# Performance work log

Measured on AMD Instinct MI355X. Metric: run time of the kernel, lower is better.

Reference implementation:

```python
import jax, jax.numpy as jnp
import numpy as np

BZ, IN_DIM, STATE_DIM, OUT_DIM, L = 16, 512, 512, 512, 2048
INIT_SCALE = 0.5


def setup_inputs() -> dict:
    key = jax.random.key(0)
    k_u, k_a, k_b, k_c = jax.random.split(key, 4)
    u = jax.random.normal(k_u, (BZ, IN_DIM, L), dtype=jnp.float32)
    A_unconstrained = jax.random.normal(k_a, (STATE_DIM,), dtype=jnp.float32) * 0.1
    B = jax.random.normal(k_b, (STATE_DIM, IN_DIM), dtype=jnp.float32) * INIT_SCALE / np.sqrt(IN_DIM)
    C = jax.random.normal(k_c, (OUT_DIM, STATE_DIM), dtype=jnp.float32) * INIT_SCALE / np.sqrt(STATE_DIM)
    D = jnp.zeros((OUT_DIM, IN_DIM), dtype=jnp.float32)
    h0 = jnp.zeros((STATE_DIM,), dtype=jnp.float32)
    return {"u": u, "A_unconstrained": A_unconstrained, "B": B, "C": C, "D": D, "h0": h0}


def reference(u, A_unconstrained, B, C, D, h0):
    # u: (Bz, input_dim, L)
    Bz = u.shape[0]
    A_diag = -jax.nn.softplus(A_unconstrained)  # (S,)
    # Time-invariant input projection, batched over all timesteps: (L, Bz, S)
    Bu = jnp.einsum('bil,si->lbs', u, B)

    state0 = jnp.broadcast_to(h0[None, :], (Bz, h0.shape[0]))

    def step(state, bu_t):
        x_t = state * A_diag[None, :] + bu_t  # (Bz, S)
        return x_t, x_t

    _, xs = jax.lax.scan(step, state0, Bu)  # xs: (L, Bz, S)

    # Output projection: y_t = C x_t + D u_t  -> (Bz, out, L)
    Y = jnp.einsum('lbs,os->bol', xs, C) + jnp.einsum('bil,oi->bol', u, D)
    return Y
```

## Files before the change

### kernel.cpp

```cpp
#include <hip/hip_runtime.h>
#include <math.h>

typedef __bf16 bf16;
typedef __bf16 bf16x2 __attribute__((ext_vector_type(2)));
typedef __bf16 bf16x4 __attribute__((ext_vector_type(4)));
typedef __bf16 bf16x8 __attribute__((ext_vector_type(8)));
typedef float  f32x4  __attribute__((ext_vector_type(4)));

#define BZd 16
#define INd 512
#define Sd  512
#define Od  512
#define Ld  2048
#define CLd 128
#define NCd (Ld / CLd)

__device__ __forceinline__ int keyf(int r) { return (r & 3) ^ ((r >> 2) & 3); }

__global__ __launch_bounds__(256) void prep_all(const float* __restrict__ B,
                                                const float* __restrict__ C,
                                                const float* __restrict__ D,
                                                const float* __restrict__ Au,
                                                bf16* __restrict__ Bb, bf16* __restrict__ Cb,
                                                bf16* __restrict__ Db, float* __restrict__ A_diag,
                                                int* __restrict__ dfa) {
    __shared__ int sred[4];
    int bid = blockIdx.x;
    if (bid == 768) {
        #pragma unroll
        for (int r = 0; r < 2; ++r) {
            int ss = threadIdx.x + r * 256;
            float x = Au[ss];
            float sp = fmaxf(x, 0.0f) + log1pf(expf(-fabsf(x)));
            A_diag[ss] = -sp;
        }
        return;
    }
    int which = bid >> 8, lb = bid & 255;
    const float* src = which == 0 ? B : (which == 1 ? C : D);
    bf16* dst = which == 0 ? Bb : (which == 1 ? Cb : Db);
    int i = lb * 256 + threadIdx.x;
    f32x4 v = *(const f32x4*)&src[(size_t)i * 4];
    bf16x4 o = { (bf16)v[0], (bf16)v[1], (bf16)v[2], (bf16)v[3] };
    *(bf16x4*)&dst[(size_t)i * 4] = o;
    if (which == 2) {
        int nz = (v[0] != 0.f) | (v[1] != 0.f) | (v[2] != 0.f) | (v[3] != 0.f);
        unsigned long long bl = __ballot(nz);
        int wv = threadIdx.x >> 6;
        if ((threadIdx.x & 63) == 0) sred[wv] = (bl != 0ull);
        __syncthreads();
        if (threadIdx.x == 0) dfa[lb] = sred[0] | sred[1] | sred[2] | sred[3];
    }
}

template<int AREG, int SCAN>
__global__ __launch_bounds__(512, 2) void gemm8p(
    const bf16* __restrict__ Abf, size_t aBS,
    const float* __restrict__ Uf, size_t uBS,
    const bf16* __restrict__ Bbf, size_t bBS,
    const bf16* __restrict__ Dbf,
    const int* __restrict__ dfa,
    const float* __restrict__ A_diag, float* __restrict__ cePtr,
    void* __restrict__ OutV, size_t oBS, int ldOut,
    int NX, int NY)
{
    constexpr int RS   = AREG ? 40 : 32;
    constexpr int ASZ  = 256 * RS;
    constexpr int SLOT = ASZ + 256 * 32;
    __shared__ bf16 lds[4 * SLOT];

    const int tid = threadIdx.x;
    const int lane = tid & 63, w = tid >> 6;

    int nwg = gridDim.x, bid = blockIdx.x;
    int cpx = nwg >> 3;
    int swz = (bid & 7) * cpx + (bid >> 3);
    int pb = NX * NY;
    int b  = swz / pb;
    int r0 = swz - b * pb;
    int by = r0 / NX;
    int bx = r0 - by * NX;

    const int wm = w >> 2, wn = w & 3;
    const int fr = lane & 15, g = lane >> 4;
    const int iq = tid & 7, lq = tid >> 3;

    const bf16*  Ab = AREG ? nullptr : (Abf + (size_t)b * aBS + (size_t)(by * 256) * 512);
    const float* Ub = Uf ? (Uf + (size_t)b * uBS) : nullptr;
    const bf16*  Bp = Bbf + (size_t)b * bBS + (size_t)(bx * 256) * 512;

    int extra = 0;
    if (!AREG && dfa) {
        int4 f = ((const int4*)dfa)[lane];
        extra = __any((f.x | f.y | f.z | f.w) != 0) ? 1 : 0;
    }

    f32x4 acc[8][4];
    #pragma unroll
    for (int i = 0; i < 8; ++i)
        #pragma unroll
        for (int j = 0; j < 4; ++j)
            acc[i][j] = (f32x4){0.f, 0.f, 0.f, 0.f};

    f32x4 areg[4];

    #define GLD16(srcP, dstElem) __builtin_amdgcn_global_load_lds( \
        (const __attribute__((address_space(1))) void*)(srcP), \
        (__attribute__((address_space(3))) void*)&lds[dstElem], 16, 0, 0)

    auto gldA = [&](int U) {
        #pragma unroll
        for (int rb = 0; rb < 2; ++rb) {
            int row = rb * 128 + (tid >> 2);
            int cs = (tid & 3) ^ keyf(row);
            GLD16(Ab + (size_t)row * 512 + U * 32 + cs * 8,
                  (U & 3) * SLOT + (rb * 128 + w * 16) * 32);
        }
    };
    auto gldB = [&](int U) {
        #pragma unroll
        for (int rb = 0; rb < 2; ++rb) {
            int row = rb * 128 + (tid >> 2);
            int cs = (tid & 3) ^ keyf(row);
            GLD16(Bp + (size_t)row * 512 + U * 32 + cs * 8,
                  (U & 3) * SLOT + ASZ + (rb * 128 + w * 16) * 32);
        }
    };
    auto issueA = [&](int U) {
        #pragma unroll
        for (int d = 0; d < 4; ++d)
            areg[d] = *(const f32x4*)&Ub[(size_t)(U * 32 + iq * 4 + d) * Ld + by * 256 + lq * 4];
    };
    auto writeA = [&](int U) {
        bf16* As = &lds[(U & 3) * SLOT];
        #pragma unroll
        for (int dl = 0; dl < 4; ++dl) {
            int r = lq * 4 + dl;
            bf16x4 wv = { (bf16)areg[0][dl], (bf16)areg[1][dl], (bf16)areg[2][dl], (bf16)areg[3][dl] };
            *(bf16x4*)&As[r * RS + iq * 4] = wv;
        }
    };
    auto readFrags = [&](int slot, bf16x8* avf, bf16x8* bvf) {
        const bf16* As = &lds[slot * SLOT];
        const bf16* Bs = &lds[slot * SLOT + ASZ];
        #pragma unroll
        for (int i = 0; i < 8; ++i) {
            int R = wm * 128 + i * 16 + fr;
            if (AREG) avf[i] = *(const bf16x8*)&As[R * RS + g * 8];
            else      avf[i] = *(const bf16x8*)&As[R * RS + (g ^ keyf(R)) * 8];
        }
        #pragma unroll
        for (int j = 0; j < 4; ++j) {
            int R = wn * 64 + j * 16 + fr;
            bvf[j] = *(const bf16x8*)&Bs[R * 32 + (g ^ keyf(R)) * 8];
        }
    };

    if (AREG) { issueA(0); gldB(0); gldB(1); }
    else      { gldA(0); gldB(0); gldA(1); gldB(1); }

    for (int U = 0; U < 16; ++U) {
        if (U < 15) {
            if (AREG) asm volatile("s_waitcnt vmcnt(2)" ::: "memory");
            else      asm volatile("s_waitcnt vmcnt(4)" ::: "memory");
        } else {
            asm volatile("s_waitcnt vmcnt(0)" ::: "memory");
        }
        __builtin_amdgcn_sched_barrier(0);
        if (AREG) {
            writeA(U);
            asm volatile("s_waitcnt lgkmcnt(0)" ::: "memory");
            __builtin_amdgcn_sched_barrier(0);
        }
        __builtin_amdgcn_s_barrier();
        __builtin_amdgcn_sched_barrier(0);
        if (AREG && U + 1 < 16) {
            issueA(U + 1);
            __builtin_amdgcn_sched_barrier(0);
        }
        bf16x8 av[8], bv[4];
        readFrags(U & 3, av, bv);
        if (!AREG && U + 2 < 16) gldA(U + 2);
        if (U + 2 < 16) gldB(U + 2);
        __builtin_amdgcn_s_setprio(1);
        #pragma unroll
        for (int i = 0; i < 8; ++i)
            #pragma unroll
            for (int j = 0; j < 4; ++j)
                acc[i][j] = __builtin_amdgcn_mfma_f32_16x16x32_bf16(av[i], bv[j], acc[i][j], 0, 0, 0);
        __builtin_amdgcn_s_setprio(0);
    }

    if (!AREG) {
        if (extra) {
            #pragma unroll 1
            for (int T = 0; T < 16; ++T) {
                int k0 = T * 32;
                __builtin_amdgcn_s_barrier();
                f32x4 r4[4];
                #pragma unroll
                for (int d = 0; d < 4; ++d)
                    r4[d] = *(const f32x4*)&Ub[(size_t)(k0 + iq * 4 + d) * Ld + bx * 256 + lq * 4];
                #pragma unroll
                for (int rb = 0; rb < 2; ++rb) {
                    int row = rb * 128 + (tid >> 2);
                    int cs = (tid & 3) ^ keyf(row);
                    GLD16(Dbf + (size_t)(by * 256 + row) * 512 + k0 + cs * 8,
                          (rb * 128 + w * 16) * 32);
                }
                asm volatile("s_waitcnt vmcnt(0)" ::: "memory");
                #pragma unroll
                for (int dl = 0; dl < 4; ++dl) {
                    int r = lq * 4 + dl;
                    bf16x4 wv = { (bf16)r4[0][dl], (bf16)r4[1][dl], (bf16)r4[2][dl], (bf16)r4[3][dl] };
                    int e = ((iq >> 1) ^ keyf(r)) * 8 + (iq & 1) * 4;
                    *(bf16x4*)&lds[ASZ + r * 32 + e] = wv;
                }
                asm volatile("s_waitcnt lgkmcnt(0)" ::: "memory");
                __builtin_amdgcn_s_barrier();
                bf16x8 av[8], bv[4];
                readFrags(0, av, bv);
                #pragma unroll
                for (int i = 0; i < 8; ++i)
                    #pragma unroll
                    for (int j = 0; j < 4; ++j)
                        acc[i][j] = __builtin_amdgcn_mfma_f32_16x16x32_bf16(av[i], bv[j], acc[i][j], 0, 0, 0);
            }
        }
    }

    int n0 = bx * 256 + wn * 64 + fr;
    int m0 = by * 256 + wm * 128 + g * 4;

    if (SCAN) {
        #pragma unroll
        for (int j = 0; j < 4; ++j) {
            float a = A_diag[n0 + j * 16];
            float a2 = a * a, a4 = a2 * a2, a8 = a4 * a4, a16 = a8 * a8;
            float S = 0.f;
            #pragma unroll
            for (int i = 0; i < 8; ++i) {
                f32x4 v = acc[i][j];
                float e = fmaf(fmaf(fmaf(v[0], a, v[1]), a, v[2]), a, v[3]);
                float e0 = __shfl(e, fr), e1 = __shfl(e, fr + 16);
                float e2 = __shfl(e, fr + 32), e3 = __shfl(e, fr + 48);
                float E = fmaf(fmaf(fmaf(e0, a4, e1), a4, e2), a4, e3);
                S = fmaf(S, a16, E);
            }
            if (g == 0)
                cePtr[((size_t)b * NCd + (by * 2 + wm)) * Sd + n0 + j * 16] = S;
        }
    }

    if (SCAN) {
        bf16* out = (bf16*)OutV + (size_t)b * oBS;
        #pragma unroll
        for (int i = 0; i < 8; ++i)
            #pragma unroll
            for (int j = 0; j < 4; ++j)
                #pragma unroll
                for (int q = 0; q < 4; ++q)
                    out[(size_t)(m0 + i * 16 + q) * ldOut + n0 + j * 16] = (bf16)acc[i][j][q];
    } else {
        float* out = (float*)OutV + (size_t)b * oBS;
        #pragma unroll
        for (int i = 0; i < 8; ++i)
            #pragma unroll
            for (int j = 0; j < 4; ++j)
                #pragma unroll
                for (int q = 0; q < 4; ++q)
                    out[(size_t)(m0 + i * 16 + q) * ldOut + n0 + j * 16] = acc[i][j][q];
    }
    #undef GLD16
}

__global__ __launch_bounds__(256) void pass_scan2(bf16* __restrict__ xbuf,
                                                  const float* __restrict__ A_diag,
                                                  const float* __restrict__ ce,
                                                  const float* __restrict__ h0) {
    int gI = blockIdx.x * 256 + threadIdx.x;
    int sp = gI & 255;
    int c = (gI >> 8) & (NCd - 1);
    int b = gI >> 12;
    int s = sp * 2;
    float a0 = A_diag[s], a1 = A_diag[s + 1];
    float acl0 = a0, acl1 = a1;
    #pragma unroll
    for (int i = 0; i < 7; ++i) { acl0 *= acl0; acl1 *= acl1; }
    float x0 = h0[s], x1 = h0[s + 1];
    for (int cp = 0; cp < NCd; ++cp) {
        if (cp >= c) break;
        float2 e = *(const float2*)&ce[((size_t)b * NCd + cp) * Sd + s];
        x0 = fmaf(acl0, x0, e.x);
        x1 = fmaf(acl1, x1, e.y);
    }
    bf16* p = xbuf + ((size_t)b * Ld + (size_t)c * CLd) * Sd + s;
    #pragma unroll 4
    for (int j = 0; j < CLd; ++j) {
        bf16x2 v = *(const bf16x2*)&p[(size_t)j * Sd];
        x0 = fmaf(a0, x0, (float)v[0]);
        x1 = fmaf(a1, x1, (float)v[1]);
        bf16x2 o = { (bf16)x0, (bf16)x1 };
        *(bf16x2*)&p[(size_t)j * Sd] = o;
    }
}

extern "C" void kernel_launch(void* const* d_in, const int* in_sizes, int n_in,
                              void* d_out, int out_size, void* d_ws, size_t ws_size,
                              hipStream_t stream) {
    const float* u  = (const float*)d_in[0];
    const float* Au = (const float*)d_in[1];
    const float* Bm = (const float*)d_in[2];
    const float* Cm = (const float*)d_in[3];
    const float* Dm = (const float*)d_in[4];
    const float* h0 = (const float*)d_in[5];
    float* Y = (float*)d_out;

    char* ws = (char*)d_ws;
    bf16* xs = (bf16*)ws;
    bf16* Bb = (bf16*)(ws + (32ull << 20));
    bf16* Cb = Bb + 262144;
    bf16* Db = Cb + 262144;
    float* A_diag = (float*)(ws + (32ull << 20) + 3ull * 524288);
    float* ce     = A_diag + 512;
    int*   dfa    = (int*)(ce + (size_t)BZd * NCd * Sd);

    prep_all<<<769, 256, 0, stream>>>(Bm, Cm, Dm, Au, Bb, Cb, Db, A_diag, dfa);

    gemm8p<1, 1><<<(Sd / 256) * (Ld / 256) * BZd, 512, 0, stream>>>(
        nullptr, 0, u, (size_t)INd * Ld, Bb, 0, nullptr,
        nullptr, A_diag, ce,
        (void*)xs, (size_t)Ld * Sd, Sd,
        Sd / 256, Ld / 256);

    pass_scan2<<<(BZd * NCd * (Sd / 2)) / 256, 256, 0, stream>>>(xs, A_diag, ce, h0);

    gemm8p<0, 0><<<(Ld / 256) * (Od / 256) * BZd, 512, 0, stream>>>(
        Cb, 0, u, (size_t)INd * Ld, xs, (size_t)Ld * Sd, Db,
        dfa, A_diag, nullptr,
        (void*)Y, (size_t)Od * Ld, Ld,
        Ld / 256, Od / 256);
}
```

Measured before the change: 87.40 us.

## Replace first-stage GEMM with dedicated 128x128-tile kernel with fused chunk scan

The input-projection GEMM (u times B) moves from the templated 256x256-tile, 512-thread kernel to a new 256-thread kernel with 128x128 tiles and 1024 workgroups. It double-buffers the register-staged A operand and triple-buffers B in LDS with swizzled A writes, and combines the two warp-row chunk summaries through LDS so one ce entry per 128-row chunk is written. The aim is more workgroups for better CU occupancy and load balance, less LDS per block, and bank-conflict-free A fragment reads. The old template loses its AREG/SCAN paths. The cost is lower per-tile reuse of B and u.

```diff
diff --git a/kernel.cpp b/kernel.cpp
--- a/kernel.cpp
+++ b/kernel.cpp
@@ -53,6 +53,165 @@
     }
 }
 
+__global__ __launch_bounds__(256, 2) void gemm_bu128(
+    const float* __restrict__ Uf,
+    const bf16* __restrict__ Bbf,
+    const float* __restrict__ A_diag,
+    float* __restrict__ ce,
+    bf16* __restrict__ xs)
+{
+    constexpr int ASLOT = 128 * 32;
+    constexpr int BSLOT = 128 * 32;
+    __shared__ bf16 lds[2 * ASLOT + 3 * BSLOT];
+
+    const int tid = threadIdx.x, lane = tid & 63, w = tid >> 6;
+
+    int nwg = gridDim.x, bid = blockIdx.x;
+    int cpx = nwg >> 3;
+    int swz = (bid & 7) * cpx + (bid >> 3);
+    int b  = swz >> 6;
+    int r0 = swz & 63;
+    int by = r0 >> 2;
+    int bx = r0 & 3;
+
+    const int wm = w >> 1, wn = w & 1;
+    const int fr = lane & 15, g = lane >> 4;
+    const int iq = tid & 7, lq = tid >> 3;
+
+    const float* Ub = Uf + (size_t)b * INd * Ld;
+    const bf16*  Bp = Bbf + (size_t)(bx * 128) * 512;
+
+    f32x4 acc[4][4];
+    #pragma unroll
+    for (int i = 0; i < 4; ++i)
+        #pragma unroll
+        for (int j = 0; j < 4; ++j)
+            acc[i][j] = (f32x4){0.f, 0.f, 0.f, 0.f};
+
+    f32x4 areg[4];
+
+    #define GLD16B(srcP, dstElem) __builtin_amdgcn_global_load_lds( \
+        (const __attribute__((address_space(1))) void*)(srcP), \
+        (__attribute__((address_space(3))) void*)&lds[dstElem], 16, 0, 0)
+
+    auto issueA = [&](int U) {
+        #pragma unroll
+        for (int d = 0; d < 4; ++d)
+            areg[d] = *(const f32x4*)&Ub[(size_t)(U * 32 + iq * 4 + d) * Ld + by * 128 + lq * 4];
+    };
+    auto writeA = [&](int U) {
+        bf16* As = &lds[(U & 1) * ASLOT];
+        #pragma unroll
+        for (int dl = 0; dl < 4; ++dl) {
+            int r = lq * 4 + dl;
+            bf16x4 wv = { (bf16)areg[0][dl], (bf16)areg[1][dl], (bf16)areg[2][dl], (bf16)areg[3][dl] };
+            *(bf16x4*)&As[r * 32 + (((iq >> 1) ^ keyf(r)) * 8) + (iq & 1) * 4] = wv;
+        }
+    };
+    auto gldB = [&](int U) {
+        #pragma unroll
+        for (int rb = 0; rb < 2; ++rb) {
+            int row = rb * 64 + (tid >> 2);
+            int cs = (tid & 3) ^ keyf(row);
+            GLD16B(Bp + (size_t)row * 512 + U * 32 + cs * 8,
+                   2 * ASLOT + (U % 3) * BSLOT + (rb * 64 + w * 16) * 32);
+        }
+    };
+
+    issueA(0);
+    __builtin_amdgcn_sched_barrier(0);
+    gldB(0); gldB(1);
+    __builtin_amdgcn_sched_barrier(0);
+
+    for (int U = 0; U < 16; ++U) {
+        if (U < 15) { asm volatile("s_waitcnt vmcnt(2)" ::: "memory"); }
+        else        { asm volatile("s_waitcnt vmcnt(0)" ::: "memory"); }
+        __builtin_amdgcn_sched_barrier(0);
+        writeA(U);
+        asm volatile("s_waitcnt lgkmcnt(0)" ::: "memory");
+        __builtin_amdgcn_sched_barrier(0);
+        __builtin_amdgcn_s_barrier();
+        __builtin_amdgcn_sched_barrier(0);
+        if (U + 1 < 16) {
+            issueA(U + 1);
+            __builtin_amdgcn_sched_barrier(0);
+        }
+        bf16x8 av[4], bv[4];
+        {
+            const bf16* As = &lds[(U & 1) * ASLOT];
+            const bf16* Bs = &lds[2 * ASLOT + (U % 3) * BSLOT];
+            #pragma unroll
+            for (int i = 0; i < 4; ++i) {
+                int R = wm * 64 + i * 16 + fr;
+                av[i] = *(const bf16x8*)&As[R * 32 + (g ^ keyf(R)) * 8];
+            }
+            #pragma unroll
+            for (int j = 0; j < 4; ++j) {
+                int R = wn * 64 + j * 16 + fr;
+                bv[j] = *(const bf16x8*)&Bs[R * 32 + (g ^ keyf(R)) * 8];
+            }
+        }
+        if (U + 2 < 16) {
+            gldB(U + 2);
+            __builtin_amdgcn_sched_barrier(0);
+        }
+        __builtin_amdgcn_s_setprio(1);
+        #pragma unroll
+        for (int i = 0; i < 4; ++i)
+            #pragma unroll
+            for (int j = 0; j < 4; ++j)
+                acc[i][j] = __builtin_amdgcn_mfma_f32_16x16x32_bf16(av[i], bv[j], acc[i][j], 0, 0, 0);
+        __builtin_amdgcn_s_setprio(0);
+    }
+
+    int n0 = bx * 128 + wn * 64 + fr;
+    int m0 = by * 128 + wm * 64 + g * 4;
+
+    __syncthreads();
+    float* scf = (float*)lds;
+    float Sv[4], a64j[4];
+    #pragma unroll
+    for (int j = 0; j < 4; ++j) {
+        float a = A_diag[n0 + j * 16];
+        float a2 = a * a, a4 = a2 * a2, a8 = a4 * a4, a16 = a8 * a8;
+        float a32 = a16 * a16;
+        a64j[j] = a32 * a32;
+        float S = 0.f;
+        #pragma unroll
+        for (int i = 0; i < 4; ++i) {
+            f32x4 v = acc[i][j];
+            float e = fmaf(fmaf(fmaf(v[0], a, v[1]), a, v[2]), a, v[3]);
+            float e0 = __shfl(e, fr), e1 = __shfl(e, fr + 16);
+            float e2 = __shfl(e, fr + 32), e3 = __shfl(e, fr + 48);
+            float E = fmaf(fmaf(fmaf(e0, a4, e1), a4, e2), a4, e3);
+            S = fmaf(S, a16, E);
+        }
+        Sv[j] = S;
+    }
+    if (wm == 0 && g == 0) {
+        #pragma unroll
+        for (int j = 0; j < 4; ++j) scf[wn * 64 + j * 16 + fr] = Sv[j];
+    }
+    __syncthreads();
+    if (wm == 1 && g == 0) {
+        #pragma unroll
+        for (int j = 0; j < 4; ++j) {
+            float S0 = scf[wn * 64 + j * 16 + fr];
+            ce[((size_t)b * NCd + by) * Sd + n0 + j * 16] = fmaf(S0, a64j[j], Sv[j]);
+        }
+    }
+
+    bf16* out = xs + (size_t)b * Ld * Sd;
+    #pragma unroll
+    for (int i = 0; i < 4; ++i)
+        #pragma unroll
+        for (int j = 0; j < 4; ++j)
+            #pragma unroll
+            for (int q = 0; q < 4; ++q)
+                out[(size_t)(m0 + i * 16 + q) * Sd + n0 + j * 16] = (bf16)acc[i][j][q];
+    #undef GLD16B
+}
+
 template<int AREG, int SCAN>
 __global__ __launch_bounds__(512, 2) void gemm8p(
     const bf16* __restrict__ Abf, size_t aBS,
@@ -64,7 +223,7 @@
     void* __restrict__ OutV, size_t oBS, int ldOut,
     int NX, int NY)
 {
-    constexpr int RS   = AREG ? 40 : 32;
+    constexpr int RS   = 32;
     constexpr int ASZ  = 256 * RS;
     constexpr int SLOT = ASZ + 256 * 32;
     __shared__ bf16 lds[4 * SLOT];
@@ -85,12 +244,12 @@
     const int fr = lane & 15, g = lane >> 4;
     const int iq = tid & 7, lq = tid >> 3;
 
-    const bf16*  Ab = AREG ? nullptr : (Abf + (size_t)b * aBS + (size_t)(by * 256) * 512);
+    const bf16*  Ab = Abf + (size_t)b * aBS + (size_t)(by * 256) * 512;
     const float* Ub = Uf ? (Uf + (size_t)b * uBS) : nullptr;
     const bf16*  Bp = Bbf + (size_t)b * bBS + (size_t)(bx * 256) * 512;
 
     int extra = 0;
-    if (!AREG && dfa) {
+    if (dfa) {
         int4 f = ((const int4*)dfa)[lane];
         extra = __any((f.x | f.y | f.z | f.w) != 0) ? 1 : 0;
     }
@@ -101,8 +260,6 @@
         #pragma unroll
         for (int j = 0; j < 4; ++j)
             acc[i][j] = (f32x4){0.f, 0.f, 0.f, 0.f};
-
-    f32x4 areg[4];
 
     #define GLD16(srcP, dstElem) __builtin_amdgcn_global_load_lds( \
         (const __attribute__((address_space(1))) void*)(srcP), \
@@ -126,28 +283,13 @@
                   (U & 3) * SLOT + ASZ + (rb * 128 + w * 16) * 32);
         }
     };
-    auto issueA = [&](int U) {
-        #pragma unroll
-        for (int d = 0; d < 4; ++d)
-            areg[d] = *(const f32x4*)&Ub[(size_t)(U * 32 + iq * 4 + d) * Ld + by * 256 + lq * 4];
-    };
-    auto writeA = [&](int U) {
-        bf16* As = &lds[(U & 3) * SLOT];
-        #pragma unroll
-        for (int dl = 0; dl < 4; ++dl) {
-            int r = lq * 4 + dl;
-            bf16x4 wv = { (bf16)areg[0][dl], (bf16)areg[1][dl], (bf16)areg[2][dl], (bf16)areg[3][dl] };
-            *(bf16x4*)&As[r * RS + iq * 4] = wv;
-        }
-    };
     auto readFrags = [&](int slot, bf16x8* avf, bf16x8* bvf) {
         const bf16* As = &lds[slot * SLOT];
         const bf16* Bs = &lds[slot * SLOT + ASZ];
         #pragma unroll
         for (int i = 0; i < 8; ++i) {
             int R = wm * 128 + i * 16 + fr;
-            if (AREG) avf[i] = *(const bf16x8*)&As[R * RS + g * 8];
-            else      avf[i] = *(const bf16x8*)&As[R * RS + (g ^ keyf(R)) * 8];
+            avf[i] = *(const bf16x8*)&As[R * RS + (g ^ keyf(R)) * 8];
         }
         #pragma unroll
         for (int j = 0; j < 4; ++j) {
@@ -156,31 +298,17 @@
         }
     };
 
-    if (AREG) { issueA(0); gldB(0); gldB(1); }
-    else      { gldA(0); gldB(0); gldA(1); gldB(1); }
+    gldA(0); gldB(0); gldA(1); gldB(1);
 
     for (int U = 0; U < 16; ++U) {
-        if (U < 15) {
-            if (AREG) asm volatile("s_waitcnt vmcnt(2)" ::: "memory");
-            else      asm volatile("s_waitcnt vmcnt(4)" ::: "memory");
-        } else {
-            asm volatile("s_waitcnt vmcnt(0)" ::: "memory");
-        }
+        if (U < 15) { asm volatile("s_waitcnt vmcnt(4)" ::: "memory"); }
+        else        { asm volatile("s_waitcnt vmcnt(0)" ::: "memory"); }
         __builtin_amdgcn_sched_barrier(0);
-        if (AREG) {
-            writeA(U);
-            asm volatile("s_waitcnt lgkmcnt(0)" ::: "memory");
-            __builtin_amdgcn_sched_barrier(0);
-        }
         __builtin_amdgcn_s_barrier();
         __builtin_amdgcn_sched_barrier(0);
-        if (AREG && U + 1 < 16) {
-            issueA(U + 1);
-            __builtin_amdgcn_sched_barrier(0);
-        }
         bf16x8 av[8], bv[4];
         readFrags(U & 3, av, bv);
-        if (!AREG && U + 2 < 16) gldA(U + 2);
+        if (U + 2 < 16) gldA(U + 2);
         if (U + 2 < 16) gldB(U + 2);
         __builtin_amdgcn_s_setprio(1);
         #pragma unroll
@@ -191,86 +319,52 @@
         __builtin_amdgcn_s_setprio(0);
     }
 
-    if (!AREG) {
-        if (extra) {
-            #pragma unroll 1
-            for (int T = 0; T < 16; ++T) {
-                int k0 = T * 32;
-                __builtin_amdgcn_s_barrier();
-                f32x4 r4[4];
+    if (extra) {
+        #pragma unroll 1
+        for (int T = 0; T < 16; ++T) {
+            int k0 = T * 32;
+            __builtin_amdgcn_s_barrier();
+            f32x4 r4[4];
+            #pragma unroll
+            for (int d = 0; d < 4; ++d)
+                r4[d] = *(const f32x4*)&Ub[(size_t)(k0 + iq * 4 + d) * Ld + bx * 256 + lq * 4];
+            #pragma unroll
+            for (int rb = 0; rb < 2; ++rb) {
+                int row = rb * 128 + (tid >> 2);
+                int cs = (tid & 3) ^ keyf(row);
+                GLD16(Dbf + (size_t)(by * 256 + row) * 512 + k0 + cs * 8,
+                      (rb * 128 + w * 16) * 32);
+            }
+            asm volatile("s_waitcnt vmcnt(0)" ::: "memory");
+            #pragma unroll
+            for (int dl = 0; dl < 4; ++dl) {
+                int r = lq * 4 + dl;
+                bf16x4 wv = { (bf16)r4[0][dl], (bf16)r4[1][dl], (bf16)r4[2][dl], (bf16)r4[3][dl] };
+                int e = ((iq >> 1) ^ keyf(r)) * 8 + (iq & 1) * 4;
+                *(bf16x4*)&lds[ASZ + r * 32 + e] = wv;
+            }
+            asm volatile("s_waitcnt lgkmcnt(0)" ::: "memory");
+            __builtin_amdgcn_s_barrier();
+            bf16x8 av[8], bv[4];
+            readFrags(0, av, bv);
+            #pragma unroll
+            for (int i = 0; i < 8; ++i)
                 #pragma unroll
-                for (int d = 0; d < 4; ++d)
-                    r4[d] = *(const f32x4*)&Ub[(size_t)(k0 + iq * 4 + d) * Ld + bx * 256 + lq * 4];
-                #pragma unroll
-                for (int rb = 0; rb < 2; ++rb) {
-                    int row = rb * 128 + (tid >> 2);
-                    int cs = (tid & 3) ^ keyf(row);
-                    GLD16(Dbf + (size_t)(by * 256 + row) * 512 + k0 + cs * 8,
-                          (rb * 128 + w * 16) * 32);
-                }
-                asm volatile("s_waitcnt vmcnt(0)" ::: "memory");
-                #pragma unroll
-                for (int dl = 0; dl < 4; ++dl) {
-                    int r = lq * 4 + dl;
-                    bf16x4 wv = { (bf16)r4[0][dl], (bf16)r4[1][dl], (bf16)r4[2][dl], (bf16)r4[3][dl] };
-                    int e = ((iq >> 1) ^ keyf(r)) * 8 + (iq & 1) * 4;
-                    *(bf16x4*)&lds[ASZ + r * 32 + e] = wv;
-                }
-                asm volatile("s_waitcnt lgkmcnt(0)" ::: "memory");
-                __builtin_amdgcn_s_barrier();
-                bf16x8 av[8], bv[4];
-                readFrags(0, av, bv);
-                #pragma unroll
-                for (int i = 0; i < 8; ++i)
-                    #pragma unroll
-                    for (int j = 0; j < 4; ++j)
-                        acc[i][j] = __builtin_amdgcn_mfma_f32_16x16x32_bf16(av[i], bv[j], acc[i][j], 0, 0, 0);
-            }
+                for (int j = 0; j < 4; ++j)
+                    acc[i][j] = __builtin_amdgcn_mfma_f32_16x16x32_bf16(av[i], bv[j], acc[i][j], 0, 0, 0);
         }
     }
 
     int n0 = bx * 256 + wn * 64 + fr;
     int m0 = by * 256 + wm * 128 + g * 4;
-
-    if (SCAN) {
-        #pragma unroll
-        for (int j = 0; j < 4; ++j) {
-            float a = A_diag[n0 + j * 16];
-            float a2 = a * a, a4 = a2 * a2, a8 = a4 * a4, a16 = a8 * a8;
-            float S = 0.f;
-            #pragma unroll
-            for (int i = 0; i < 8; ++i) {
-                f32x4 v = acc[i][j];
-                float e = fmaf(fmaf(fmaf(v[0], a, v[1]), a, v[2]), a, v[3]);
-                float e0 = __shfl(e, fr), e1 = __shfl(e, fr + 16);
-                float e2 = __shfl(e, fr + 32), e3 = __shfl(e, fr + 48);
-                float E = fmaf(fmaf(fmaf(e0, a4, e1), a4, e2), a4, e3);
-                S = fmaf(S, a16, E);
-            }
-            if (g == 0)
-                cePtr[((size_t)b * NCd + (by * 2 + wm)) * Sd + n0 + j * 16] = S;
-        }
-    }
-
-    if (SCAN) {
-        bf16* out = (bf16*)OutV + (size_t)b * oBS;
-        #pragma unroll
-        for (int i = 0; i < 8; ++i)
-            #pragma unroll
-            for (int j = 0; j < 4; ++j)
-                #pragma unroll
-                for (int q = 0; q < 4; ++q)
-                    out[(size_t)(m0 + i * 16 + q) * ldOut + n0 + j * 16] = (bf16)acc[i][j][q];
-    } else {
-        float* out = (float*)OutV + (size_t)b * oBS;
-        #pragma unroll
-        for (int i = 0; i < 8; ++i)
-            #pragma unroll
-            for (int j = 0; j < 4; ++j)
-                #pragma unroll
-                for (int q = 0; q < 4; ++q)
-                    out[(size_t)(m0 + i * 16 + q) * ldOut + n0 + j * 16] = acc[i][j][q];
-    }
+    float* out = (float*)OutV + (size_t)b * oBS;
+    #pragma unroll
+    for (int i = 0; i < 8; ++i)
+        #pragma unroll
+        for (int j = 0; j < 4; ++j)
+            #pragma unroll
+            for (int q = 0; q < 4; ++q)
+                out[(size_t)(m0 + i * 16 + q) * ldOut + n0 + j * 16] = acc[i][j][q];
     #undef GLD16
 }
 
@@ -327,11 +421,7 @@
 
     prep_all<<<769, 256, 0, stream>>>(Bm, Cm, Dm, Au, Bb, Cb, Db, A_diag, dfa);
 
-    gemm8p<1, 1><<<(Sd / 256) * (Ld / 256) * BZd, 512, 0, stream>>>(
-        nullptr, 0, u, (size_t)INd * Ld, Bb, 0, nullptr,
-        nullptr, A_diag, ce,
-        (void*)xs, (size_t)Ld * Sd, Sd,
-        Sd / 256, Ld / 256);
+    gemm_bu128<<<1024, 256, 0, stream>>>(u, Bb, A_diag, ce, xs);
 
     pass_scan2<<<(BZd * NCd * (Sd / 2)) / 256, 256, 0, stream>>>(xs, A_diag, ce, h0);
 
```

Measured after the change: 100.3 us. +14.7%, slower.

## Pre-transpose u to bf16 and load GEMM1 A operand via direct LDS loads

Applied to the files above, without the earlier changes.

Adds a separate kernel that transposes u from (B, I, L) fp32 into an (B, L, I) bf16 buffer in workspace. The first GEMM then streams this operand with the same async global-to-LDS path as the second GEMM, instead of loading fp32 into registers, converting and writing to LDS in the main loop. This removes per-iteration register staging, conversion and the extra LDS-write wait from the GEMM pipeline. In exchange it adds an extra kernel launch plus a full read of u and a 32 MB bf16 write and re-read.

```diff
diff --git a/kernel.cpp b/kernel.cpp
--- a/kernel.cpp
+++ b/kernel.cpp
@@ -53,7 +53,36 @@
     }
 }
 
-template<int AREG, int SCAN>
+__global__ __launch_bounds__(256) void transp_u(const float* __restrict__ u,
+                                                bf16* __restrict__ ut) {
+    __shared__ bf16 t[64][73];
+    int b = blockIdx.z, i0 = blockIdx.y * 64, l0 = blockIdx.x * 64;
+    int tid = threadIdx.x, tx = tid & 15, ty = tid >> 4;
+    const float* ub = u + ((size_t)b * INd + i0) * Ld + l0;
+    #pragma unroll
+    for (int r = 0; r < 4; ++r) {
+        int il = r * 16 + ty;
+        float4 v = *(const float4*)&ub[(size_t)il * Ld + tx * 4];
+        t[il][tx * 4 + 0] = (bf16)v.x;
+        t[il][tx * 4 + 1] = (bf16)v.y;
+        t[il][tx * 4 + 2] = (bf16)v.z;
+        t[il][tx * 4 + 3] = (bf16)v.w;
+    }
+    __syncthreads();
+    bf16* uo = ut + ((size_t)b * Ld + l0) * INd + i0;
+    #pragma unroll
+    for (int it = 0; it < 2; ++it) {
+        int q = it * 256 + tid;
+        int lr = q >> 3;
+        int ic = (q & 7) * 8;
+        bf16x8 o;
+        #pragma unroll
+        for (int e = 0; e < 8; ++e) o[e] = t[ic + e][lr];
+        *(bf16x8*)&uo[(size_t)lr * INd + ic] = o;
+    }
+}
+
+template<int SCAN>
 __global__ __launch_bounds__(512, 2) void gemm8p(
     const bf16* __restrict__ Abf, size_t aBS,
     const float* __restrict__ Uf, size_t uBS,
@@ -64,7 +93,7 @@
     void* __restrict__ OutV, size_t oBS, int ldOut,
     int NX, int NY)
 {
-    constexpr int RS   = AREG ? 40 : 32;
+    constexpr int RS   = 32;
     constexpr int ASZ  = 256 * RS;
     constexpr int SLOT = ASZ + 256 * 32;
     __shared__ bf16 lds[4 * SLOT];
@@ -85,12 +114,12 @@
     const int fr = lane & 15, g = lane >> 4;
     const int iq = tid & 7, lq = tid >> 3;
 
-    const bf16*  Ab = AREG ? nullptr : (Abf + (size_t)b * aBS + (size_t)(by * 256) * 512);
+    const bf16*  Ab = Abf + (size_t)b * aBS + (size_t)(by * 256) * 512;
     const float* Ub = Uf ? (Uf + (size_t)b * uBS) : nullptr;
     const bf16*  Bp = Bbf + (size_t)b * bBS + (size_t)(bx * 256) * 512;
 
     int extra = 0;
-    if (!AREG && dfa) {
+    if (!SCAN && dfa) {
         int4 f = ((const int4*)dfa)[lane];
         extra = __any((f.x | f.y | f.z | f.w) != 0) ? 1 : 0;
     }
@@ -101,8 +130,6 @@
         #pragma unroll
         for (int j = 0; j < 4; ++j)
             acc[i][j] = (f32x4){0.f, 0.f, 0.f, 0.f};
-
-    f32x4 areg[4];
 
     #define GLD16(srcP, dstElem) __builtin_amdgcn_global_load_lds( \
         (const __attribute__((address_space(1))) void*)(srcP), \
@@ -126,28 +153,13 @@
                   (U & 3) * SLOT + ASZ + (rb * 128 + w * 16) * 32);
         }
     };
-    auto issueA = [&](int U) {
-        #pragma unroll
-        for (int d = 0; d < 4; ++d)
-            areg[d] = *(const f32x4*)&Ub[(size_t)(U * 32 + iq * 4 + d) * Ld + by * 256 + lq * 4];
-    };
-    auto writeA = [&](int U) {
-        bf16* As = &lds[(U & 3) * SLOT];
-        #pragma unroll
-        for (int dl = 0; dl < 4; ++dl) {
-            int r = lq * 4 + dl;
-            bf16x4 wv = { (bf16)areg[0][dl], (bf16)areg[1][dl], (bf16)areg[2][dl], (bf16)areg[3][dl] };
-            *(bf16x4*)&As[r * RS + iq * 4] = wv;
-        }
-    };
     auto readFrags = [&](int slot, bf16x8* avf, bf16x8* bvf) {
         const bf16* As = &lds[slot * SLOT];
         const bf16* Bs = &lds[slot * SLOT + ASZ];
         #pragma unroll
         for (int i = 0; i < 8; ++i) {
             int R = wm * 128 + i * 16 + fr;
-            if (AREG) avf[i] = *(const bf16x8*)&As[R * RS + g * 8];
-            else      avf[i] = *(const bf16x8*)&As[R * RS + (g ^ keyf(R)) * 8];
+            avf[i] = *(const bf16x8*)&As[R * RS + (g ^ keyf(R)) * 8];
         }
         #pragma unroll
         for (int j = 0; j < 4; ++j) {
@@ -156,31 +168,17 @@
         }
     };
 
-    if (AREG) { issueA(0); gldB(0); gldB(1); }
-    else      { gldA(0); gldB(0); gldA(1); gldB(1); }
+    gldA(0); gldB(0); gldA(1); gldB(1);
 
     for (int U = 0; U < 16; ++U) {
-        if (U < 15) {
-            if (AREG) asm volatile("s_waitcnt vmcnt(2)" ::: "memory");
-            else      asm volatile("s_waitcnt vmcnt(4)" ::: "memory");
-        } else {
-            asm volatile("s_waitcnt vmcnt(0)" ::: "memory");
-        }
+        if (U < 15) { asm volatile("s_waitcnt vmcnt(4)" ::: "memory"); }
+        else        { asm volatile("s_waitcnt vmcnt(0)" ::: "memory"); }
         __builtin_amdgcn_sched_barrier(0);
-        if (AREG) {
-            writeA(U);
-            asm volatile("s_waitcnt lgkmcnt(0)" ::: "memory");
-            __builtin_amdgcn_sched_barrier(0);
-        }
         __builtin_amdgcn_s_barrier();
         __builtin_amdgcn_sched_barrier(0);
-        if (AREG && U + 1 < 16) {
-            issueA(U + 1);
-            __builtin_amdgcn_sched_barrier(0);
-        }
         bf16x8 av[8], bv[4];
         readFrags(U & 3, av, bv);
-        if (!AREG && U + 2 < 16) gldA(U + 2);
+        if (U + 2 < 16) gldA(U + 2);
         if (U + 2 < 16) gldB(U + 2);
         __builtin_amdgcn_s_setprio(1);
         #pragma unroll
@@ -191,41 +189,39 @@
         __builtin_amdgcn_s_setprio(0);
     }
 
-    if (!AREG) {
-        if (extra) {
-            #pragma unroll 1
-            for (int T = 0; T < 16; ++T) {
-                int k0 = T * 32;
-                __builtin_amdgcn_s_barrier();
-                f32x4 r4[4];
+    if (!SCAN && extra) {
+        #pragma unroll 1
+        for (int T = 0; T < 16; ++T) {
+            int k0 = T * 32;
+            __builtin_amdgcn_s_barrier();
+            f32x4 r4[4];
+            #pragma unroll
+            for (int d = 0; d < 4; ++d)
+                r4[d] = *(const f32x4*)&Ub[(size_t)(k0 + iq * 4 + d) * Ld + bx * 256 + lq * 4];
+            #pragma unroll
+            for (int rb = 0; rb < 2; ++rb) {
+                int row = rb * 128 + (tid >> 2);
+                int cs = (tid & 3) ^ keyf(row);
+                GLD16(Dbf + (size_t)(by * 256 + row) * 512 + k0 + cs * 8,
+                      (rb * 128 + w * 16) * 32);
+            }
+            asm volatile("s_waitcnt vmcnt(0)" ::: "memory");
+            #pragma unroll
+            for (int dl = 0; dl < 4; ++dl) {
+                int r = lq * 4 + dl;
+                bf16x4 wv = { (bf16)r4[0][dl], (bf16)r4[1][dl], (bf16)r4[2][dl], (bf16)r4[3][dl] };
+                int e = ((iq >> 1) ^ keyf(r)) * 8 + (iq & 1) * 4;
+                *(bf16x4*)&lds[ASZ + r * 32 + e] = wv;
+            }
+            asm volatile("s_waitcnt lgkmcnt(0)" ::: "memory");
+            __builtin_amdgcn_s_barrier();
+            bf16x8 av[8], bv[4];
+            readFrags(0, av, bv);
+            #pragma unroll
+            for (int i = 0; i < 8; ++i)
                 #pragma unroll
-                for (int d = 0; d < 4; ++d)
-                    r4[d] = *(const f32x4*)&Ub[(size_t)(k0 + iq * 4 + d) * Ld + bx * 256 + lq * 4];
-                #pragma unroll
-                for (int rb = 0; rb < 2; ++rb) {
-                    int row = rb * 128 + (tid >> 2);
-                    int cs = (tid & 3) ^ keyf(row);
-                    GLD16(Dbf + (size_t)(by * 256 + row) * 512 + k0 + cs * 8,
-                          (rb * 128 + w * 16) * 32);
-                }
-                asm volatile("s_waitcnt vmcnt(0)" ::: "memory");
-                #pragma unroll
-                for (int dl = 0; dl < 4; ++dl) {
-                    int r = lq * 4 + dl;
-                    bf16x4 wv = { (bf16)r4[0][dl], (bf16)r4[1][dl], (bf16)r4[2][dl], (bf16)r4[3][dl] };
-                    int e = ((iq >> 1) ^ keyf(r)) * 8 + (iq & 1) * 4;
-                    *(bf16x4*)&lds[ASZ + r * 32 + e] = wv;
-                }
-                asm volatile("s_waitcnt lgkmcnt(0)" ::: "memory");
-                __builtin_amdgcn_s_barrier();
-                bf16x8 av[8], bv[4];
-                readFrags(0, av, bv);
-                #pragma unroll
-                for (int i = 0; i < 8; ++i)
-                    #pragma unroll
-                    for (int j = 0; j < 4; ++j)
-                        acc[i][j] = __builtin_amdgcn_mfma_f32_16x16x32_bf16(av[i], bv[j], acc[i][j], 0, 0, 0);
-            }
+                for (int j = 0; j < 4; ++j)
+                    acc[i][j] = __builtin_amdgcn_mfma_f32_16x16x32_bf16(av[i], bv[j], acc[i][j], 0, 0, 0);
         }
     }
 
@@ -318,24 +314,26 @@
 
     char* ws = (char*)d_ws;
     bf16* xs = (bf16*)ws;
-    bf16* Bb = (bf16*)(ws + (32ull << 20));
+    bf16* ut = (bf16*)(ws + (32ull << 20));
+    bf16* Bb = (bf16*)(ws + (64ull << 20));
     bf16* Cb = Bb + 262144;
     bf16* Db = Cb + 262144;
-    float* A_diag = (float*)(ws + (32ull << 20) + 3ull * 524288);
+    float* A_diag = (float*)(ws + (64ull << 20) + 3ull * 524288);
     float* ce     = A_diag + 512;
     int*   dfa    = (int*)(ce + (size_t)BZd * NCd * Sd);
 
     prep_all<<<769, 256, 0, stream>>>(Bm, Cm, Dm, Au, Bb, Cb, Db, A_diag, dfa);
-
-    gemm8p<1, 1><<<(Sd / 256) * (Ld / 256) * BZd, 512, 0, stream>>>(
-        nullptr, 0, u, (size_t)INd * Ld, Bb, 0, nullptr,
+    transp_u<<<dim3(Ld / 64, INd / 64, BZd), 256, 0, stream>>>(u, ut);
+
+    gemm8p<1><<<(Sd / 256) * (Ld / 256) * BZd, 512, 0, stream>>>(
+        ut, (size_t)Ld * INd, nullptr, 0, Bb, 0, nullptr,
         nullptr, A_diag, ce,
         (void*)xs, (size_t)Ld * Sd, Sd,
         Sd / 256, Ld / 256);
 
     pass_scan2<<<(BZd * NCd * (Sd / 2)) / 256, 256, 0, stream>>>(xs, A_diag, ce, h0);
 
-    gemm8p<0, 0><<<(Ld / 256) * (Od / 256) * BZd, 512, 0, stream>>>(
+    gemm8p<0><<<(Ld / 256) * (Od / 256) * BZd, 512, 0, stream>>>(
         Cb, 0, u, (size_t)INd * Ld, xs, (size_t)Ld * Sd, Db,
         dfa, A_diag, nullptr,
         (void*)Y, (size_t)Od * Ld, Ld,
```

Result: slower. 94.35 us (+8.0%).
